# Kernel optimization log

Measured on AMD Instinct MI355X. Metric: run time of the kernel, lower is better.

## Reference

```python
import jax, jax.numpy as jnp
import numpy as np


def setup_inputs() -> dict:
    key = jax.random.key(0)
    ks = jax.random.split(key, 6)
    B, S, D_IN, D_OUT, E, R = 4, 2048, 4096, 4096, 8, 16
    x = jax.random.normal(ks[0], (B, S, D_IN), dtype=jnp.float32)
    probs = jax.random.uniform(ks[1], (B, E), dtype=jnp.float32)
    router_probs = probs / jnp.sum(probs, axis=-1, keepdims=True)
    weight = jax.random.normal(ks[2], (D_OUT, D_IN), dtype=jnp.float32) * 0.02
    bias = jax.random.normal(ks[3], (D_OUT,), dtype=jnp.float32) * 0.02
    lora_A = jax.random.normal(ks[4], (E, R, D_IN), dtype=jnp.float32) * 0.02
    lora_B = jax.random.normal(ks[5], (E, D_OUT, R), dtype=jnp.float32) * 0.02
    return {"x": x, "router_probs": router_probs, "weight": weight,
            "bias": bias, "lora_A": lora_A, "lora_B": lora_B}


def reference(x, router_probs, weight, bias, lora_A, lora_B):
    scaling = 2.0
    # base linear: [b,s,i] @ [o,i]^T + bias
    base_out = jnp.einsum('bsi,oi->bso', x, weight) + bias
    # low-rank per-expert projection: [b,s,e,r] (small: r=16)
    mid = jnp.einsum('bsi,eri->bser', x, lora_A)
    # weight by router probs (per batch, per expert) before up-projection
    mid_w = mid * router_probs[:, None, :, None]
    # sum over experts fused into the up-projection contraction
    delta = jnp.einsum('bser,eor->bso', mid_w, lora_B) * scaling
    return base_out + delta
```

## Files before the change

### kernel.cpp

```cpp
#include <hip/hip_runtime.h>


typedef _Float16 half8 __attribute__((ext_vector_type(8)));
typedef _Float16 half4 __attribute__((ext_vector_type(4)));
typedef float    f32x4 __attribute__((ext_vector_type(4)));

#define M_TOT 8192
#define N_TOT 4096
#define K_IN  4096
#define KA    4224
#define NT    66

__device__ __forceinline__ void cvt_store4(_Float16* p, float4 f) {
  half4 h;
  h[0] = (_Float16)f.x; h[1] = (_Float16)f.y;
  h[2] = (_Float16)f.z; h[3] = (_Float16)f.w;
  *(half4*)p = h;
}

template <int LOG2C, int DCOLS>
__global__ __launch_bounds__(256) void convert_f32_f16_t(
    const float* __restrict__ src, _Float16* __restrict__ dst, int total8) {
  for (int i = blockIdx.x * 256 + threadIdx.x; i < total8;
       i += gridDim.x * 256) {
    int base = i << 3;
    int r = base >> LOG2C;
    int c = base & ((1 << LOG2C) - 1);
    const float4* s = (const float4*)(src + (size_t)base);
    float4 f0 = s[0], f1 = s[1];
    half8 h;
    h[0]=(_Float16)f0.x; h[1]=(_Float16)f0.y; h[2]=(_Float16)f0.z; h[3]=(_Float16)f0.w;
    h[4]=(_Float16)f1.x; h[5]=(_Float16)f1.y; h[6]=(_Float16)f1.z; h[7]=(_Float16)f1.w;
    *(half8*)(dst + (size_t)r * DCOLS + c) = h;
  }
}

__global__ __launch_bounds__(256) void wtail_gather_f16(
    const float* __restrict__ loraB, _Float16* __restrict__ Wa) {
  int idx = blockIdx.x * 256 + threadIdx.x;
  int n = idx >> 7, j = idx & 127;
  int e = j >> 4, r = j & 15;
  Wa[(size_t)n * KA + K_IN + j] =
      (_Float16)loraB[((size_t)e * N_TOT + n) * 16 + r];
}

__global__ __launch_bounds__(256) void lorabf_gather_f32(
    const float* __restrict__ loraB, float* __restrict__ lorabf) {
  int idx = blockIdx.x * 256 + threadIdx.x;
  int n = idx >> 7, j = idx & 127;
  int e = j >> 4, r = j & 15;
  lorabf[(size_t)n * 128 + j] = loraB[((size_t)e * N_TOT + n) * 16 + r];
}

__global__ __launch_bounds__(256) void mid2_kernel(
    _Float16* __restrict__ Xa, const _Float16* __restrict__ lAh,
    const float* __restrict__ router) {
  __shared__ _Float16 As[32 * 64];
  __shared__ _Float16 Bs[128 * 64];
  int tid = threadIdx.x, lane = tid & 63, w = tid >> 6;
  int m0 = blockIdx.x * 32;
  int b = m0 >> 11;
  f32x4 acc[2][2] = {};

  for (int ks = 0; ks < 64; ++ks) {
    int kb = ks * 128;
    {
      const char* s = (const char*)Xa +
          (size_t)(m0 + w * 8 + (lane >> 3)) * (KA * 2) + kb + (lane & 7) * 16;
      __builtin_amdgcn_global_load_lds(
          (const __attribute__((address_space(1))) void*)s,
          (__attribute__((address_space(3))) void*)((char*)As + w * 1024), 16, 0, 0);
    }
#pragma unroll
    for (int i = 0; i < 4; ++i) {
      const char* s = (const char*)lAh +
          (size_t)((w * 4 + i) * 8 + (lane >> 3)) * (4096 * 2) + kb + (lane & 7) * 16;
      __builtin_amdgcn_global_load_lds(
          (const __attribute__((address_space(1))) void*)s,
          (__attribute__((address_space(3))) void*)((char*)Bs + (w * 4 + i) * 1024), 16, 0, 0);
    }
    __syncthreads();
#pragma unroll
    for (int kk = 0; kk < 2; ++kk) {
      half8 a[2], bf[2];
#pragma unroll
      for (int mi = 0; mi < 2; ++mi)
        a[mi] = *(const half8*)(As + (mi * 16 + (lane & 15)) * 64 + kk * 32 + (lane >> 4) * 8);
#pragma unroll
      for (int ni = 0; ni < 2; ++ni)
        bf[ni] = *(const half8*)(Bs + (w * 32 + ni * 16 + (lane & 15)) * 64 + kk * 32 + (lane >> 4) * 8);
#pragma unroll
      for (int mi = 0; mi < 2; ++mi)
#pragma unroll
        for (int ni = 0; ni < 2; ++ni)
          acc[mi][ni] = __builtin_amdgcn_mfma_f32_16x16x32_f16(a[mi], bf[ni], acc[mi][ni], 0, 0, 0);
    }
    __syncthreads();
  }

#pragma unroll
  for (int ni = 0; ni < 2; ++ni) {
    int j = w * 32 + ni * 16 + (lane & 15);
    int e = j >> 4;
    float sc = 2.0f * router[b * 8 + e];
#pragma unroll
    for (int mi = 0; mi < 2; ++mi) {
      f32x4 v = acc[mi][ni];
#pragma unroll
      for (int jj = 0; jj < 4; ++jj) {
        int m = m0 + mi * 16 + (lane >> 4) * 4 + jj;
        Xa[(size_t)m * KA + K_IN + j] = (_Float16)(v[jj] * sc);
      }
    }
  }
}

__global__ __launch_bounds__(256) void mid_kernel(
    const float* __restrict__ x, const float* __restrict__ loraA,
    const float* __restrict__ router, float* __restrict__ midw) {
  __shared__ _Float16 As[32 * 64];
  __shared__ _Float16 Bs[128 * 64];
  int tid = threadIdx.x, lane = tid & 63, w = tid >> 6;
  int m0 = blockIdx.x * 32;
  int b = m0 >> 11;
  f32x4 acc[2][2] = {};
  for (int ks = 0; ks < 64; ++ks) {
    int k0 = ks * 64;
#pragma unroll
    for (int it = 0; it < 2; ++it) {
      int idx = tid + it * 256;
      int r = idx >> 4, c4 = idx & 15;
      float4 f = *(const float4*)(x + (size_t)(m0 + r) * K_IN + k0 + c4 * 4);
      cvt_store4(As + r * 64 + c4 * 4, f);
    }
#pragma unroll
    for (int it = 0; it < 8; ++it) {
      int idx = tid + it * 256;
      int r = idx >> 4, c4 = idx & 15;
      float4 f = *(const float4*)(loraA + (size_t)r * K_IN + k0 + c4 * 4);
      cvt_store4(Bs + r * 64 + c4 * 4, f);
    }
    __syncthreads();
#pragma unroll
    for (int kk = 0; kk < 2; ++kk) {
      half8 a[2], bf[2];
#pragma unroll
      for (int mi = 0; mi < 2; ++mi)
        a[mi] = *(const half8*)(As + (mi * 16 + (lane & 15)) * 64 + kk * 32 + (lane >> 4) * 8);
#pragma unroll
      for (int ni = 0; ni < 2; ++ni)
        bf[ni] = *(const half8*)(Bs + (w * 32 + ni * 16 + (lane & 15)) * 64 + kk * 32 + (lane >> 4) * 8);
#pragma unroll
      for (int mi = 0; mi < 2; ++mi)
#pragma unroll
        for (int ni = 0; ni < 2; ++ni)
          acc[mi][ni] = __builtin_amdgcn_mfma_f32_16x16x32_f16(a[mi], bf[ni], acc[mi][ni], 0, 0, 0);
    }
    __syncthreads();
  }
#pragma unroll
  for (int ni = 0; ni < 2; ++ni) {
    int j = w * 32 + ni * 16 + (lane & 15);
    int e = j >> 4;
    float sc = 2.0f * router[b * 8 + e];
#pragma unroll
    for (int mi = 0; mi < 2; ++mi) {
      f32x4 v = acc[mi][ni];
#pragma unroll
      for (int jj = 0; jj < 4; ++jj) {
        int m = m0 + mi * 16 + (lane >> 4) * 4 + jj;
        midw[(size_t)m * 128 + j] = v[jj] * sc;
      }
    }
  }
}

#define BAR   __builtin_amdgcn_s_barrier()
#define PRIO1 __builtin_amdgcn_s_setprio(1)
#define PRIO0 __builtin_amdgcn_s_setprio(0)
#define LGKM0 do { asm volatile("s_waitcnt lgkmcnt(0)" ::: "memory"); \
                   __builtin_amdgcn_sched_barrier(0); } while (0)
#define VMW4  asm volatile("s_waitcnt vmcnt(4)" ::: "memory")
#define VMW2  asm volatile("s_waitcnt vmcnt(2)" ::: "memory")
#define VMW0  asm volatile("s_waitcnt vmcnt(0)" ::: "memory")
#define GLOAD(src, dst) __builtin_amdgcn_global_load_lds( \
    (const __attribute__((address_space(1))) void*)(src), \
    (__attribute__((address_space(3))) void*)(dst), 16, 0, 0)

#define LOAD_A(mb, buf) do { \
  _Pragma("unroll") for (int mi = 0; mi < 4; ++mi) { \
    int row = wm + ((mb) + mi) * 16 + ln15; \
    _Pragma("unroll") for (int kk = 0; kk < 2; ++kk) \
      areg[mi][kk] = *(const half8*)((const char*)(buf) + row * 128 + \
                                     (((kk * 4 + ln4) ^ ln7) * 16)); \
  } } while (0)

#define LOAD_B(nb, buf) do { \
  _Pragma("unroll") for (int ni = 0; ni < 2; ++ni) { \
    int row = wn + ((nb) + ni) * 16 + ln15; \
    _Pragma("unroll") for (int kk = 0; kk < 2; ++kk) \
      breg[ni][kk] = *(const half8*)((const char*)(buf) + row * 128 + \
                                     (((kk * 4 + ln4) ^ ln7) * 16)); \
  } } while (0)

#define MFMA_Q(mb, nb) do { \
  _Pragma("unroll") for (int kk = 0; kk < 2; ++kk) \
    _Pragma("unroll") for (int mi = 0; mi < 4; ++mi) \
      _Pragma("unroll") for (int ni = 0; ni < 2; ++ni) \
        acc[(mb) + mi][(nb) + ni] = __builtin_amdgcn_mfma_f32_16x16x32_f16( \
            areg[mi][kk], breg[ni][kk], acc[(mb) + mi][(nb) + ni], 0, 0, 0); \
  } while (0)

__global__ __launch_bounds__(512, 2) void gemm256(
    const _Float16* __restrict__ Xa, const _Float16* __restrict__ Wa,
    const float* __restrict__ bias, float* __restrict__ out) {
  __shared__ _Float16 As[2][256 * 64];
  __shared__ _Float16 Bs[2][256 * 64];

  int tid = threadIdx.x, lane = tid & 63, w = tid >> 6;
  int ln15 = lane & 15, ln4 = lane >> 4, ln7 = lane & 7;
  int wm = (w >> 2) * 128, wn = (w & 3) * 64;

  int bid = blockIdx.x;
  int swz = (bid & 7) * 64 + (bid >> 3);
  int nt = swz >> 5, mt = swz & 31;
  int m0 = mt << 8, n0 = nt << 8;

  const char* XpC = (const char*)Xa + (size_t)m0 * (KA * 2);
  const char* WpC = (const char*)Wa + (size_t)n0 * (KA * 2);

  int lrow = lane >> 3;
  int scol = ((lane & 7) ^ lrow) * 16;
  int offA1[2], offA3[2], offB1[2], offB2[2];
  int ldsA1[2], ldsA3[2], ldsB1[2], ldsB2[2];
#pragma unroll
  for (int j = 0; j < 2; ++j) {
    int g = 2 * w + j;
    int rA = (g >> 3) * 128 + (g & 7) * 8;
    offA1[j] = (rA + lrow) * (KA * 2) + scol;      ldsA1[j] = rA * 128;
    int rA3 = rA + 64;
    offA3[j] = (rA3 + lrow) * (KA * 2) + scol;     ldsA3[j] = rA3 * 128;
    int rB = (g >> 2) * 64 + (g & 3) * 8;
    offB1[j] = (rB + lrow) * (KA * 2) + scol;      ldsB1[j] = rB * 128;
    int rB2 = rB + 32;
    offB2[j] = (rB2 + lrow) * (KA * 2) + scol;     ldsB2[j] = rB2 * 128;
  }

  f32x4 acc[8][4] = {};
  half8 areg[4][2], breg[2][2];

  {
    char* nA = (char*)&As[0][0]; char* nB = (char*)&Bs[0][0];
    GLOAD(XpC + offA1[0], nA + ldsA1[0]); GLOAD(XpC + offA1[1], nA + ldsA1[1]);
    GLOAD(WpC + offB1[0], nB + ldsB1[0]); GLOAD(WpC + offB1[1], nB + ldsB1[1]);
    GLOAD(WpC + offB2[0], nB + ldsB2[0]); GLOAD(WpC + offB2[1], nB + ldsB2[1]);
    GLOAD(XpC + offA3[0], nA + ldsA3[0]); GLOAD(XpC + offA3[1], nA + ldsA3[1]);
    VMW0; BAR;
  }

#pragma unroll 1
  for (int t = 0; t < NT - 1; ++t) {
    const _Float16* cA = As[t & 1];
    const _Float16* cB = Bs[t & 1];
    char* nA = (char*)&As[(t + 1) & 1][0];
    char* nB = (char*)&Bs[(t + 1) & 1][0];
    const char* sA = XpC + (size_t)(t + 1) * 128;
    const char* sB = WpC + (size_t)(t + 1) * 128;

    LOAD_A(0, cA); LOAD_B(0, cB);
    GLOAD(sA + offA1[0], nA + ldsA1[0]); GLOAD(sA + offA1[1], nA + ldsA1[1]);
    BAR; LGKM0; PRIO1; MFMA_Q(0, 0); PRIO0; VMW4; BAR;
    LOAD_B(2, cB);
    GLOAD(sB + offB1[0], nB + ldsB1[0]); GLOAD(sB + offB1[1], nB + ldsB1[1]);
    BAR; LGKM0; PRIO1; MFMA_Q(0, 2); PRIO0; VMW4; BAR;
    LOAD_A(4, cA);
    GLOAD(sB + offB2[0], nB + ldsB2[0]); GLOAD(sB + offB2[1], nB + ldsB2[1]);
    BAR; LGKM0; PRIO1; MFMA_Q(4, 2); PRIO0; BAR;
    LOAD_B(0, cB);
    GLOAD(sA + offA3[0], nA + ldsA3[0]); GLOAD(sA + offA3[1], nA + ldsA3[1]);
    BAR; LGKM0; PRIO1; MFMA_Q(4, 0); PRIO0; VMW4; BAR;
  }

  {
    const _Float16* cA = As[(NT - 1) & 1];
    const _Float16* cB = Bs[(NT - 1) & 1];
    LOAD_A(0, cA); LOAD_B(0, cB);
    BAR; LGKM0; PRIO1; MFMA_Q(0, 0); PRIO0; VMW2; BAR;
    LOAD_B(2, cB);
    BAR; LGKM0; PRIO1; MFMA_Q(0, 2); PRIO0; VMW0; BAR;
    LOAD_A(4, cA);
    BAR; LGKM0; PRIO1; MFMA_Q(4, 2); PRIO0; BAR;
    LOAD_B(0, cB);
    BAR; LGKM0; PRIO1; MFMA_Q(4, 0); PRIO0;
  }

#pragma unroll
  for (int ni = 0; ni < 4; ++ni) {
    int n = n0 + wn + ni * 16 + ln15;
    float bz = bias[n];
#pragma unroll
    for (int mi = 0; mi < 8; ++mi) {
      f32x4 v = acc[mi][ni];
      int mb = m0 + wm + mi * 16 + ln4 * 4;
#pragma unroll
      for (int jj = 0; jj < 4; ++jj)
        out[(size_t)(mb + jj) * N_TOT + n] = v[jj] + bz;
    }
  }
}

__global__ __launch_bounds__(256) void gemm_fallback(
    const float* __restrict__ x, const float* __restrict__ wgt,
    const float* __restrict__ midw, const float* __restrict__ lorabf,
    const float* __restrict__ bias, float* __restrict__ out) {
  __shared__ _Float16 As[128 * 64];
  __shared__ _Float16 Bs[128 * 64];
  int tid = threadIdx.x, lane = tid & 63, w = tid >> 6;
  int mt = blockIdx.x & 63, nt = blockIdx.x >> 6;
  int m0 = mt << 7, n0 = nt << 7;
  int wm = (w >> 1) * 64, wn = (w & 1) * 64;
  f32x4 acc[4][4] = {};
  for (int ks = 0; ks < NT; ++ks) {
    int k0 = ks * 64;
    const float *asrc, *bsrc; size_t astr, bstr; int ac, bc;
    if (ks < 64) { asrc = x;    astr = K_IN; ac = k0;        bsrc = wgt;    bstr = K_IN; bc = k0; }
    else         { asrc = midw; astr = 128;  ac = k0 - K_IN; bsrc = lorabf; bstr = 128;  bc = k0 - K_IN; }
#pragma unroll
    for (int it = 0; it < 8; ++it) {
      int idx = tid + it * 256;
      int r = idx >> 4, c4 = idx & 15;
      float4 fa = *(const float4*)(asrc + (size_t)(m0 + r) * astr + ac + c4 * 4);
      cvt_store4(As + r * 64 + c4 * 4, fa);
      float4 fb = *(const float4*)(bsrc + (size_t)(n0 + r) * bstr + bc + c4 * 4);
      cvt_store4(Bs + r * 64 + c4 * 4, fb);
    }
    __syncthreads();
#pragma unroll
    for (int kk = 0; kk < 2; ++kk) {
      half8 a[4], bf[4];
#pragma unroll
      for (int mi = 0; mi < 4; ++mi)
        a[mi] = *(const half8*)(As + (wm + mi * 16 + (lane & 15)) * 64 + kk * 32 + (lane >> 4) * 8);
#pragma unroll
      for (int ni = 0; ni < 4; ++ni)
        bf[ni] = *(const half8*)(Bs + (wn + ni * 16 + (lane & 15)) * 64 + kk * 32 + (lane >> 4) * 8);
#pragma unroll
      for (int mi = 0; mi < 4; ++mi)
#pragma unroll
        for (int ni = 0; ni < 4; ++ni)
          acc[mi][ni] = __builtin_amdgcn_mfma_f32_16x16x32_f16(a[mi], bf[ni], acc[mi][ni], 0, 0, 0);
    }
    __syncthreads();
  }
#pragma unroll
  for (int ni = 0; ni < 4; ++ni) {
    int n = n0 + wn + ni * 16 + (lane & 15);
    float bz = bias[n];
#pragma unroll
    for (int mi = 0; mi < 4; ++mi) {
      f32x4 v = acc[mi][ni];
      int mbase = m0 + wm + mi * 16 + (lane >> 4) * 4;
#pragma unroll
      for (int jj = 0; jj < 4; ++jj)
        out[(size_t)(mbase + jj) * N_TOT + n] = v[jj] + bz;
    }
  }
}

extern "C" void kernel_launch(void* const* d_in, const int* in_sizes, int n_in,
                              void* d_out, int out_size, void* d_ws, size_t ws_size,
                              hipStream_t stream) {
  const float* x      = (const float*)d_in[0];
  const float* router = (const float*)d_in[1];
  const float* wgt    = (const float*)d_in[2];
  const float* bias   = (const float*)d_in[3];
  const float* loraA  = (const float*)d_in[4];
  const float* loraB  = (const float*)d_in[5];
  float* out = (float*)d_out;
  char* ws = (char*)d_ws;

  const size_t XAUG_B = (size_t)M_TOT * KA * 2;
  const size_t WAUG_B = (size_t)N_TOT * KA * 2;
  const size_t LAH_B  = (size_t)128 * K_IN * 2;
  const size_t MIDW_B = (size_t)M_TOT * 128 * 4;
  bool fast = ws_size >= XAUG_B + WAUG_B + LAH_B;

  if (fast) {
    _Float16* Xa  = (_Float16*)ws;
    _Float16* Wa  = (_Float16*)(ws + XAUG_B);
    _Float16* lAh = (_Float16*)(ws + XAUG_B + WAUG_B);
    convert_f32_f16_t<12, KA><<<2048, 256, 0, stream>>>(x,   Xa, M_TOT * K_IN / 8);
    convert_f32_f16_t<12, KA><<<2048, 256, 0, stream>>>(wgt, Wa, N_TOT * K_IN / 8);
    convert_f32_f16_t<12, 4096><<<256, 256, 0, stream>>>(loraA, lAh, 128 * K_IN / 8);
    wtail_gather_f16<<<2048, 256, 0, stream>>>(loraB, Wa);
    mid2_kernel<<<256, 256, 0, stream>>>(Xa, lAh, router);
    gemm256<<<512, 512, 0, stream>>>(Xa, Wa, bias, out);
  } else {
    float* midw   = (float*)ws;
    float* lorabf = (float*)(ws + MIDW_B);
    lorabf_gather_f32<<<2048, 256, 0, stream>>>(loraB, lorabf);
    mid_kernel<<<256, 256, 0, stream>>>(x, loraA, router, midw);
    gemm_fallback<<<2048, 256, 0, stream>>>(x, wgt, midw, lorabf, bias, out);
  }
}
```

Baseline: 443.5 us.

## Restructure GEMM main loop pipeline with A prefetched two stages ahead and full B register caching

Reworks the 256x256 GEMM main loop so the A tile is prefetched two k-steps ahead into the buffer just consumed, while B is prefetched one step ahead. All four B fragments are now kept in registers, which removes the redundant B reload in the last quarter. Loop trip count, prologue and epilogue are adjusted to match. The workgroup-to-tile mapping also changes to a 2D XCD-aware grouping meant to improve L2 reuse. This raises register pressure and relies on delicate wait/barrier ordering for correctness.

```diff
diff --git a/kernel.cpp b/kernel.cpp
--- a/kernel.cpp
+++ b/kernel.cpp
@@ -180,8 +180,8 @@
 #define PRIO0 __builtin_amdgcn_s_setprio(0)
 #define LGKM0 do { asm volatile("s_waitcnt lgkmcnt(0)" ::: "memory"); \
                    __builtin_amdgcn_sched_barrier(0); } while (0)
+#define LGKM8 asm volatile("s_waitcnt lgkmcnt(8)" ::: "memory")
 #define VMW4  asm volatile("s_waitcnt vmcnt(4)" ::: "memory")
-#define VMW2  asm volatile("s_waitcnt vmcnt(2)" ::: "memory")
 #define VMW0  asm volatile("s_waitcnt vmcnt(0)" ::: "memory")
 #define GLOAD(src, dst) __builtin_amdgcn_global_load_lds( \
     (const __attribute__((address_space(1))) void*)(src), \
@@ -195,11 +195,11 @@
                                      (((kk * 4 + ln4) ^ ln7) * 16)); \
   } } while (0)
 
-#define LOAD_B(nb, buf) do { \
+#define LOAD_B2(nb, buf) do { \
   _Pragma("unroll") for (int ni = 0; ni < 2; ++ni) { \
     int row = wn + ((nb) + ni) * 16 + ln15; \
     _Pragma("unroll") for (int kk = 0; kk < 2; ++kk) \
-      breg[ni][kk] = *(const half8*)((const char*)(buf) + row * 128 + \
+      breg[(nb) + ni][kk] = *(const half8*)((const char*)(buf) + row * 128 + \
                                      (((kk * 4 + ln4) ^ ln7) * 16)); \
   } } while (0)
 
@@ -208,7 +208,7 @@
     _Pragma("unroll") for (int mi = 0; mi < 4; ++mi) \
       _Pragma("unroll") for (int ni = 0; ni < 2; ++ni) \
         acc[(mb) + mi][(nb) + ni] = __builtin_amdgcn_mfma_f32_16x16x32_f16( \
-            areg[mi][kk], breg[ni][kk], acc[(mb) + mi][(nb) + ni], 0, 0, 0); \
+            areg[mi][kk], breg[(nb) + ni][kk], acc[(mb) + mi][(nb) + ni], 0, 0, 0); \
   } while (0)
 
 __global__ __launch_bounds__(512, 2) void gemm256(
@@ -222,8 +222,9 @@
   int wm = (w >> 2) * 128, wn = (w & 3) * 64;
 
   int bid = blockIdx.x;
-  int swz = (bid & 7) * 64 + (bid >> 3);
-  int nt = swz >> 5, mt = swz & 31;
+  int xcd = bid & 7, idx = bid >> 3;
+  int mt = (xcd & 3) * 8 + (idx & 7);
+  int nt = (xcd >> 2) * 8 + (idx >> 3);
   int m0 = mt << 8, n0 = nt << 8;
 
   const char* XpC = (const char*)Xa + (size_t)m0 * (KA * 2);
@@ -231,67 +232,79 @@
 
   int lrow = lane >> 3;
   int scol = ((lane & 7) ^ lrow) * 16;
-  int offA1[2], offA3[2], offB1[2], offB2[2];
-  int ldsA1[2], ldsA3[2], ldsB1[2], ldsB2[2];
-#pragma unroll
-  for (int j = 0; j < 2; ++j) {
-    int g = 2 * w + j;
-    int rA = (g >> 3) * 128 + (g & 7) * 8;
-    offA1[j] = (rA + lrow) * (KA * 2) + scol;      ldsA1[j] = rA * 128;
-    int rA3 = rA + 64;
-    offA3[j] = (rA3 + lrow) * (KA * 2) + scol;     ldsA3[j] = rA3 * 128;
-    int rB = (g >> 2) * 64 + (g & 3) * 8;
-    offB1[j] = (rB + lrow) * (KA * 2) + scol;      ldsB1[j] = rB * 128;
-    int rB2 = rB + 32;
-    offB2[j] = (rB2 + lrow) * (KA * 2) + scol;     ldsB2[j] = rB2 * 128;
-  }
+  int off[2][2], lds_off[2][2];
+#pragma unroll
+  for (int h = 0; h < 2; ++h)
+#pragma unroll
+    for (int j = 0; j < 2; ++j) {
+      int rbase = h * 128 + w * 16 + j * 8;
+      off[h][j] = (rbase + lrow) * (KA * 2) + scol;
+      lds_off[h][j] = rbase * 128;
+    }
 
   f32x4 acc[8][4] = {};
-  half8 areg[4][2], breg[2][2];
+  half8 areg[4][2], breg[4][2];
 
   {
-    char* nA = (char*)&As[0][0]; char* nB = (char*)&Bs[0][0];
-    GLOAD(XpC + offA1[0], nA + ldsA1[0]); GLOAD(XpC + offA1[1], nA + ldsA1[1]);
-    GLOAD(WpC + offB1[0], nB + ldsB1[0]); GLOAD(WpC + offB1[1], nB + ldsB1[1]);
-    GLOAD(WpC + offB2[0], nB + ldsB2[0]); GLOAD(WpC + offB2[1], nB + ldsB2[1]);
-    GLOAD(XpC + offA3[0], nA + ldsA3[0]); GLOAD(XpC + offA3[1], nA + ldsA3[1]);
-    VMW0; BAR;
+    char* a0 = (char*)&As[0][0]; char* b0 = (char*)&Bs[0][0];
+    char* a1 = (char*)&As[1][0];
+    const char* sA1 = XpC + 128;
+    GLOAD(XpC + off[0][0], a0 + lds_off[0][0]); GLOAD(XpC + off[0][1], a0 + lds_off[0][1]);
+    GLOAD(XpC + off[1][0], a0 + lds_off[1][0]); GLOAD(XpC + off[1][1], a0 + lds_off[1][1]);
+    GLOAD(WpC + off[0][0], b0 + lds_off[0][0]); GLOAD(WpC + off[0][1], b0 + lds_off[0][1]);
+    GLOAD(WpC + off[1][0], b0 + lds_off[1][0]); GLOAD(WpC + off[1][1], b0 + lds_off[1][1]);
+    GLOAD(sA1 + off[0][0], a1 + lds_off[0][0]); GLOAD(sA1 + off[0][1], a1 + lds_off[0][1]);
+    GLOAD(sA1 + off[1][0], a1 + lds_off[1][0]); GLOAD(sA1 + off[1][1], a1 + lds_off[1][1]);
+    VMW4; BAR;
   }
 
 #pragma unroll 1
-  for (int t = 0; t < NT - 1; ++t) {
+  for (int t = 0; t < NT - 2; ++t) {
     const _Float16* cA = As[t & 1];
     const _Float16* cB = Bs[t & 1];
-    char* nA = (char*)&As[(t + 1) & 1][0];
     char* nB = (char*)&Bs[(t + 1) & 1][0];
-    const char* sA = XpC + (size_t)(t + 1) * 128;
+    char* nA = (char*)&As[t & 1][0];
     const char* sB = WpC + (size_t)(t + 1) * 128;
-
-    LOAD_A(0, cA); LOAD_B(0, cB);
-    GLOAD(sA + offA1[0], nA + ldsA1[0]); GLOAD(sA + offA1[1], nA + ldsA1[1]);
-    BAR; LGKM0; PRIO1; MFMA_Q(0, 0); PRIO0; VMW4; BAR;
-    LOAD_B(2, cB);
-    GLOAD(sB + offB1[0], nB + ldsB1[0]); GLOAD(sB + offB1[1], nB + ldsB1[1]);
-    BAR; LGKM0; PRIO1; MFMA_Q(0, 2); PRIO0; VMW4; BAR;
-    LOAD_A(4, cA);
-    GLOAD(sB + offB2[0], nB + ldsB2[0]); GLOAD(sB + offB2[1], nB + ldsB2[1]);
-    BAR; LGKM0; PRIO1; MFMA_Q(4, 2); PRIO0; BAR;
-    LOAD_B(0, cB);
-    GLOAD(sA + offA3[0], nA + ldsA3[0]); GLOAD(sA + offA3[1], nA + ldsA3[1]);
-    BAR; LGKM0; PRIO1; MFMA_Q(4, 0); PRIO0; VMW4; BAR;
-  }
-
-  {
-    const _Float16* cA = As[(NT - 1) & 1];
-    const _Float16* cB = Bs[(NT - 1) & 1];
-    LOAD_A(0, cA); LOAD_B(0, cB);
-    BAR; LGKM0; PRIO1; MFMA_Q(0, 0); PRIO0; VMW2; BAR;
-    LOAD_B(2, cB);
-    BAR; LGKM0; PRIO1; MFMA_Q(0, 2); PRIO0; VMW0; BAR;
+    const char* sA = XpC + (size_t)(t + 2) * 128;
+
+    LOAD_A(0, cA); LOAD_B2(0, cB);
+    GLOAD(sB + off[0][0], nB + lds_off[0][0]); GLOAD(sB + off[0][1], nB + lds_off[0][1]);
+    LGKM8; BAR; LGKM0; PRIO1; MFMA_Q(0, 0); PRIO0; BAR;
+    LOAD_B2(2, cB);
+    GLOAD(sB + off[1][0], nB + lds_off[1][0]); GLOAD(sB + off[1][1], nB + lds_off[1][1]);
+    BAR; LGKM0; PRIO1; MFMA_Q(0, 2); PRIO0; BAR;
     LOAD_A(4, cA);
     BAR; LGKM0; PRIO1; MFMA_Q(4, 2); PRIO0; BAR;
-    LOAD_B(0, cB);
-    BAR; LGKM0; PRIO1; MFMA_Q(4, 0); PRIO0;
+    GLOAD(sA + off[0][0], nA + lds_off[0][0]); GLOAD(sA + off[0][1], nA + lds_off[0][1]);
+    GLOAD(sA + off[1][0], nA + lds_off[1][0]); GLOAD(sA + off[1][1], nA + lds_off[1][1]);
+    BAR; PRIO1; MFMA_Q(4, 0); PRIO0; VMW4; BAR;
+  }
+
+  {
+    const _Float16* cA = As[0];
+    const _Float16* cB = Bs[0];
+    char* nB = (char*)&Bs[1][0];
+    const char* sB = WpC + (size_t)65 * 128;
+    LOAD_A(0, cA); LOAD_B2(0, cB);
+    GLOAD(sB + off[0][0], nB + lds_off[0][0]); GLOAD(sB + off[0][1], nB + lds_off[0][1]);
+    LGKM8; BAR; LGKM0; PRIO1; MFMA_Q(0, 0); PRIO0; BAR;
+    LOAD_B2(2, cB);
+    GLOAD(sB + off[1][0], nB + lds_off[1][0]); GLOAD(sB + off[1][1], nB + lds_off[1][1]);
+    BAR; LGKM0; PRIO1; MFMA_Q(0, 2); PRIO0; BAR;
+    LOAD_A(4, cA);
+    BAR; LGKM0; PRIO1; MFMA_Q(4, 2); PRIO0; BAR;
+    BAR; PRIO1; MFMA_Q(4, 0); PRIO0; VMW0; BAR;
+  }
+  {
+    const _Float16* cA = As[1];
+    const _Float16* cB = Bs[1];
+    LOAD_A(0, cA); LOAD_B2(0, cB);
+    BAR; LGKM0; PRIO1; MFMA_Q(0, 0); PRIO0; BAR;
+    LOAD_B2(2, cB);
+    BAR; LGKM0; PRIO1; MFMA_Q(0, 2); PRIO0; BAR;
+    LOAD_A(4, cA);
+    BAR; LGKM0; PRIO1; MFMA_Q(4, 2); PRIO0; BAR;
+    PRIO1; MFMA_Q(4, 0); PRIO0;
   }
 
 #pragma unroll
```

New measurement: 384.4 us. 1.15x faster.
